# Kernel tuning notes

Measured on AMD Instinct MI355X. Metric: run time of the kernel, lower is better.

Reference implementation:

```python
import jax, jax.numpy as jnp
import numpy as np

N_NODES = 50000


def setup_inputs() -> dict:
    key = jax.random.key(0)
    k1, k2, k3, k4 = jax.random.split(key, 4)
    N, E, D_IN, D_OUT = N_NODES, 1_600_000, 128, 128
    x = jax.random.normal(k1, (N, D_IN), dtype=jnp.float32)
    edge_index = jax.random.randint(k2, (2, E), 0, N, dtype=jnp.int64)
    W = jax.random.normal(k3, (D_IN, D_OUT), dtype=jnp.float32) * (1.0 / np.sqrt(D_IN))
    b = jax.random.normal(k4, (D_OUT,), dtype=jnp.float32) * 0.01
    return {"x": x, "edge_index": edge_index, "W": W, "b": b}


def reference(x, edge_index, W, b):
    N = x.shape[0]
    # add self loops: edge (i, i) for every node
    loops = jnp.arange(N, dtype=edge_index.dtype)
    row = jnp.concatenate([edge_index[0], loops])  # [E+N]
    col = jnp.concatenate([edge_index[1], loops])  # [E+N]
    # degree over col (matches torch_geometric degree(col, N))
    deg = jax.ops.segment_sum(jnp.ones_like(col, dtype=x.dtype), col, num_segments=N)
    deg_inv_sqrt = jnp.where(deg > 0, jax.lax.rsqrt(jnp.maximum(deg, 1.0)), 0.0)
    norm = deg_inv_sqrt[row] * deg_inv_sqrt[col]  # [E+N]
    # linear transform then gather-multiply-scatter (segment sum over row)
    xl = x @ W + b  # [N, D_OUT]
    msg = norm[:, None] * xl[col]  # [E+N, D_OUT]
    out = jax.ops.segment_sum(msg, row, num_segments=N)
    return out
```

## Files before the change

kernel.cpp:

```cpp
#include <hip/hip_runtime.h>
#include <hip/hip_bf16.h>


#define D     128
#define TILE  8192
#define BINB  1024
#define RPB   128
#define MAXB  512
#define SPLIT_CAP 8192

typedef short  bf16x8 __attribute__((ext_vector_type(8)));
typedef float  f32x4  __attribute__((ext_vector_type(4)));
typedef unsigned short us4 __attribute__((ext_vector_type(4)));
typedef unsigned short us8 __attribute__((ext_vector_type(8)));

static __device__ __forceinline__ unsigned short f2bf(float f) {
    unsigned u = __float_as_uint(f);
    u = (u + 0x7FFFu + ((u >> 16) & 1u)) >> 16;
    return (unsigned short)u;
}
static __device__ __forceinline__ float bf2f(unsigned short s) {
    return __uint_as_float(((unsigned)s) << 16);
}

__global__ __launch_bounds__(256) void k_prep(const float* __restrict__ W,
                                              unsigned short* __restrict__ wtb,
                                              int* __restrict__ bcur,
                                              int* __restrict__ bcurC,
                                              int NB, int CAP, int CAPC) {
    int i = blockIdx.x * 256 + threadIdx.x;
    if (i < NB) { bcur[i] = i * CAP; bcurC[i] = i * CAPC; }
    if (i < D * D) {
        int n = i >> 7, k = i & 127;
        wtb[n * 128 + k] = f2bf(W[k * 128 + n]);
    }
}

__global__ __launch_bounds__(1024) void k_binjoint(
        const int* __restrict__ rows, const int* __restrict__ cols,
        int* __restrict__ bcur, int* __restrict__ bcurC,
        unsigned* __restrict__ ebuf, unsigned char* __restrict__ cebuf,
        const float* __restrict__ x, const unsigned short* __restrict__ wtb,
        const float* __restrict__ bia, unsigned short* __restrict__ xlb,
        int E, int N, int NB, int CAP, int CAPC, int NT) {
    __shared__ __align__(16) unsigned char smem[65536];
    const int t = threadIdx.x;

    if ((int)blockIdx.x >= NT) {
        unsigned short (*wt)[136] = (unsigned short (*)[136])smem;
        unsigned short (*xs)[136] = (unsigned short (*)[136])(smem + 34816);
        const int row0 = ((int)blockIdx.x - NT) * 64;
        #pragma unroll
        for (int i = 0; i < 2; ++i) {
            int j = i * 1024 + t;
            int n = j >> 4, k8 = j & 15;
            us8 v = *(const us8*)&wtb[j * 8];
            *(us8*)&wt[n][k8 * 8] = v;
        }
        #pragma unroll
        for (int i = 0; i < 2; ++i) {
            int j = i * 1024 + t;
            int r = j >> 5, c4 = j & 31;
            int gr = row0 + r;
            us4 o = (us4){0, 0, 0, 0};
            if (gr < N) {
                float4 v = *(const float4*)&x[(size_t)gr * D + c4 * 4];
                o = (us4){f2bf(v.x), f2bf(v.y), f2bf(v.z), f2bf(v.w)};
            }
            *(us4*)&xs[r][c4 * 4] = o;
        }
        __syncthreads();
        if (t < 256) {
            const int w  = t >> 6, l = t & 63;
            const int m0 = w * 16;
            const int lm = l & 15, lq = l >> 4;
            f32x4 acc[8];
            #pragma unroll
            for (int nt = 0; nt < 8; ++nt) acc[nt] = (f32x4){0.f, 0.f, 0.f, 0.f};
            #pragma unroll
            for (int kk = 0; kk < 4; ++kk) {
                const int kof = kk * 32 + lq * 8;
                bf16x8 a = *(const bf16x8*)&xs[m0 + lm][kof];
                #pragma unroll
                for (int nt = 0; nt < 8; ++nt) {
                    bf16x8 bb = *(const bf16x8*)&wt[nt * 16 + lm][kof];
                    acc[nt] = __builtin_amdgcn_mfma_f32_16x16x32_bf16(a, bb, acc[nt], 0, 0, 0);
                }
            }
            #pragma unroll
            for (int nt = 0; nt < 8; ++nt) {
                const int col = nt * 16 + lm;
                const float bc = bia[col];
                #pragma unroll
                for (int r = 0; r < 4; ++r) {
                    int grow = row0 + m0 + lq * 4 + r;
                    if (grow < N) xlb[(size_t)grow * D + col] = f2bf(acc[nt][r] + bc);
                }
            }
        }
        return;
    }

    unsigned*       sorted  = (unsigned*)smem;
    unsigned short* sortedC = (unsigned short*)(smem + 32768);
    int* lcnt   = (int*)(smem + 49152);
    int* lbase  = lcnt + 512;
    int* excl   = lcnt + 1024;
    int* cur    = lcnt + 1536;
    int* lcntC  = lcnt + 2048;
    int* lbaseC = lcnt + 2560;
    int* exclC  = lcnt + 3072;
    int* curC   = lcnt + 3584;

    const int base = blockIdx.x * TILE;
    int m = E - base; if (m > TILE) m = TILE;

    unsigned p[TILE / BINB];
    unsigned short q[TILE / BINB];
    #pragma unroll
    for (int it = 0; it < TILE / BINB; ++it) {
        int i = it * BINB + t;
        if (i < m) {
            unsigned r = (unsigned)rows[base + i];
            unsigned c = (unsigned)cols[base + i];
            p[it] = c | ((r & 127u) << 16) | ((r >> 7) << 23);
            q[it] = (unsigned short)c;
        }
    }
    if (t < 512) { lcnt[t] = 0; lcntC[t] = 0; }
    __syncthreads();
    #pragma unroll
    for (int it = 0; it < TILE / BINB; ++it) {
        int i = it * BINB + t;
        if (i < m) {
            atomicAdd(&lcnt[p[it] >> 23], 1);
            atomicAdd(&lcntC[q[it] >> 7], 1);
        }
    }
    __syncthreads();
    if (t < 64) {
        int k0 = t * 8, v[8], s = 0;
        #pragma unroll
        for (int u = 0; u < 8; ++u) { v[u] = lcnt[k0 + u]; s += v[u]; }
        int inc = s;
        #pragma unroll
        for (int off = 1; off < 64; off <<= 1) { int o = __shfl_up(inc, off); if (t >= off) inc += o; }
        int run = inc - s;
        #pragma unroll
        for (int u = 0; u < 8; ++u) { excl[k0 + u] = run; cur[k0 + u] = run; run += v[u]; }
    } else if (t < 128) {
        int l = t - 64, k0 = l * 8, v[8], s = 0;
        #pragma unroll
        for (int u = 0; u < 8; ++u) { v[u] = lcntC[k0 + u]; s += v[u]; }
        int inc = s;
        #pragma unroll
        for (int off = 1; off < 64; off <<= 1) { int o = __shfl_up(inc, off); if (l >= off) inc += o; }
        int run = inc - s;
        #pragma unroll
        for (int u = 0; u < 8; ++u) { exclC[k0 + u] = run; curC[k0 + u] = run; run += v[u]; }
    }
    for (int b = t; b < NB; b += BINB) {
        int c = lcnt[b];
        lbase[b] = c ? atomicAdd(&bcur[b], c) : 0;
        int cc = lcntC[b];
        lbaseC[b] = cc ? atomicAdd(&bcurC[b], cc) : 0;
    }
    __syncthreads();
    #pragma unroll
    for (int it = 0; it < TILE / BINB; ++it) {
        int i = it * BINB + t;
        if (i < m) {
            int pos  = atomicAdd(&cur[p[it] >> 23], 1);
            sorted[pos] = p[it];
            int posC = atomicAdd(&curC[q[it] >> 7], 1);
            sortedC[posC] = q[it];
        }
    }
    __syncthreads();
    #pragma unroll
    for (int it = 0; it < TILE / BINB; ++it) {
        int i = it * BINB + t;
        if (i < m) {
            unsigned pp = sorted[i];
            int bk = pp >> 23;
            int g  = lbase[bk] + i - excl[bk];
            if (g < (bk + 1) * CAP) ebuf[g] = pp & 0x7FFFFFu;
            unsigned short qq = sortedC[i];
            int bc = qq >> 7;
            int gc = lbaseC[bc] + i - exclC[bc];
            if (gc < (bc + 1) * CAPC) cebuf[gc] = (unsigned char)(qq & 127u);
        }
    }
}

__global__ __launch_bounds__(1024) void k_split(const int* __restrict__ bcur,
                                                const int* __restrict__ bcurC,
                                                const unsigned* __restrict__ ebuf,
                                                const unsigned char* __restrict__ cebuf,
                                                unsigned short* __restrict__ ecol,
                                                int* __restrict__ begN,
                                                int* __restrict__ endN,
                                                float* __restrict__ dis,
                                                int N, int CAP, int CAPC) {
    __shared__ unsigned short sorted[SPLIT_CAP];
    __shared__ int cnt[RPB];
    __shared__ int excl[RPB];
    __shared__ int cur[RPB];
    __shared__ int cntD[RPB];
    const int b = blockIdx.x, t = threadIdx.x;
    const int base = b * CAP;
    int m = bcur[b] - base; if (m > CAP) m = CAP;
    const int baseC = b * CAPC;
    int mD = bcurC[b] - baseC; if (mD > CAPC) mD = CAPC;
    if (t < RPB) { cnt[t] = 0; cntD[t] = 0; }
    __syncthreads();
    const unsigned* cw = (const unsigned*)(cebuf + baseC);
    int nw = mD >> 2;
    for (int i = t; i < nw; i += 1024) {
        unsigned u = cw[i];
        atomicAdd(&cntD[u & 255u], 1);
        atomicAdd(&cntD[(u >> 8) & 255u], 1);
        atomicAdd(&cntD[(u >> 16) & 255u], 1);
        atomicAdd(&cntD[u >> 24], 1);
    }
    if (t < (mD & 3)) atomicAdd(&cntD[cebuf[baseC + nw * 4 + t]], 1);
    for (int i = t; i < m; i += 1024)
        atomicAdd(&cnt[(ebuf[base + i] >> 16) & 127], 1);
    __syncthreads();
    const int row0 = b * RPB;
    if (t < RPB && row0 + t < N)
        dis[row0 + t] = rsqrtf((float)(cntD[t] + 1));
    if (t < 64) {
        int v0 = cnt[2 * t], v1 = cnt[2 * t + 1];
        int s = v0 + v1, inc = s;
        #pragma unroll
        for (int off = 1; off < 64; off <<= 1) { int o = __shfl_up(inc, off); if (t >= off) inc += o; }
        int ex = inc - s;
        excl[2 * t] = ex;          cur[2 * t] = ex;
        excl[2 * t + 1] = ex + v0; cur[2 * t + 1] = ex + v0;
    }
    __syncthreads();
    if (t < RPB && row0 + t < N) {
        begN[row0 + t] = base + excl[t];
        endN[row0 + t] = base + excl[t] + cnt[t];
    }
    for (int i = t; i < m; i += 1024) {
        unsigned p = ebuf[base + i];
        int pos = atomicAdd(&cur[(p >> 16) & 127], 1);
        sorted[pos] = (unsigned short)(p & 0xFFFFu);
    }
    __syncthreads();
    for (int i = t; i < m; i += 1024)
        ecol[base + i] = sorted[i];
}

__global__ __launch_bounds__(256) void k_reduce(const int* __restrict__ begN,
                                                const int* __restrict__ endN,
                                                const unsigned short* __restrict__ ecol,
                                                const float* __restrict__ dis,
                                                const unsigned short* __restrict__ xlb,
                                                float* __restrict__ out, int N) {
    const int wave = threadIdx.x >> 6;
    const int lane = threadIdx.x & 63;
    const int i = blockIdx.x * 4 + wave;
    if (i >= N) return;
    const float di = dis[i];

    const ushort2 sv = *reinterpret_cast<const ushort2*>(xlb + (size_t)i * D + lane * 2);
    float ax = di * di * bf2f(sv.x);
    float ay = di * di * bf2f(sv.y);

    const int beg = begN[i], end = endN[i];
    for (int base = beg; base < end; base += 64) {
        int m = end - base; if (m > 64) m = 64;
        int   c = 0;
        float n = 0.0f;
        if (lane < m) {
            c = ecol[base + lane];
            n = di * dis[c];
        }
        for (int j = 0; j < m; j += 8) {
            float vx[8], vy[8], nn[8];
            #pragma unroll
            for (int u = 0; u < 8; ++u) {
                int cc = __shfl(c, j + u);
                ushort2 s = *reinterpret_cast<const ushort2*>(xlb + (size_t)cc * D + lane * 2);
                vx[u] = bf2f(s.x);
                vy[u] = bf2f(s.y);
                nn[u] = __shfl(n, j + u);
            }
            #pragma unroll
            for (int u = 0; u < 8; ++u) {
                ax = fmaf(nn[u], vx[u], ax);
                ay = fmaf(nn[u], vy[u], ay);
            }
        }
    }
    *reinterpret_cast<float2*>(out + (size_t)i * D + lane * 2) = make_float2(ax, ay);
}

__global__ __launch_bounds__(256) void k_zero(int* __restrict__ p, int n) {
    int i = blockIdx.x * 256 + threadIdx.x;
    if (i < n) p[i] = 0;
}
__global__ __launch_bounds__(256) void k_deg(const int* __restrict__ cols,
                                             int* __restrict__ cntc, int E) {
    int e = blockIdx.x * 256 + threadIdx.x;
    if (e < E) atomicAdd(&cntc[cols[e]], 1);
}
__global__ __launch_bounds__(256) void k_dis(const int* __restrict__ cntc,
                                             float* __restrict__ dis, int N) {
    int i = blockIdx.x * 256 + threadIdx.x;
    if (i < N) dis[i] = rsqrtf((float)(cntc[i] + 1));
}
#define GEMM_R 8
__global__ __launch_bounds__(128) void k_gemmf(const float* __restrict__ x,
                                               const float* __restrict__ W,
                                               const float* __restrict__ b,
                                               float* __restrict__ xl, int N) {
    __shared__ float xs[GEMM_R][D];
    const int c  = threadIdx.x;
    const int r0 = blockIdx.x * GEMM_R;
    #pragma unroll
    for (int r = 0; r < GEMM_R; ++r) {
        int row = r0 + r;
        xs[r][c] = (row < N) ? x[row * D + c] : 0.0f;
    }
    __syncthreads();
    float acc[GEMM_R];
    const float bc = b[c];
    #pragma unroll
    for (int r = 0; r < GEMM_R; ++r) acc[r] = bc;
    for (int k = 0; k < D; k += 4) {
        const float w0 = W[(k + 0) * D + c];
        const float w1 = W[(k + 1) * D + c];
        const float w2 = W[(k + 2) * D + c];
        const float w3 = W[(k + 3) * D + c];
        #pragma unroll
        for (int r = 0; r < GEMM_R; ++r) {
            const float4 xv = *reinterpret_cast<const float4*>(&xs[r][k]);
            acc[r] = fmaf(xv.x, w0, acc[r]);
            acc[r] = fmaf(xv.y, w1, acc[r]);
            acc[r] = fmaf(xv.z, w2, acc[r]);
            acc[r] = fmaf(xv.w, w3, acc[r]);
        }
    }
    #pragma unroll
    for (int r = 0; r < GEMM_R; ++r) {
        int row = r0 + r;
        if (row < N) xl[row * D + c] = acc[r];
    }
}
__global__ __launch_bounds__(256) void k_self(const float* __restrict__ xl,
                                              const float* __restrict__ dis,
                                              float* __restrict__ out, int N) {
    int gid = blockIdx.x * 256 + threadIdx.x;
    int i = gid >> 7;
    if (i < N) {
        float d = dis[i];
        out[gid] = d * d * xl[gid];
    }
}
__global__ __launch_bounds__(256) void k_scatter(const int* __restrict__ rows,
                                                 const int* __restrict__ cols,
                                                 const float* __restrict__ dis,
                                                 const float* __restrict__ xl,
                                                 float* __restrict__ out, int E) {
    long long gid = (long long)blockIdx.x * 256 + threadIdx.x;
    int e    = (int)(gid >> 6);
    int lane = (int)(gid & 63);
    if (e >= E) return;
    const int row = rows[e];
    const int col = cols[e];
    const float nrm = dis[row] * dis[col];
    atomicAdd(&out[row * D + lane],      nrm * xl[col * D + lane]);
    atomicAdd(&out[row * D + 64 + lane], nrm * xl[col * D + 64 + lane]);
}

extern "C" void kernel_launch(void* const* d_in, const int* in_sizes, int n_in,
                              void* d_out, int out_size, void* d_ws, size_t ws_size,
                              hipStream_t stream) {
    const float* x   = (const float*)d_in[0];
    const int*   ei  = (const int*)d_in[1];
    const float* W   = (const float*)d_in[2];
    const float* b   = (const float*)d_in[3];
    float*       out = (float*)d_out;

    const int N = in_sizes[0] / D;
    const int E = in_sizes[1] / 2;
    const int* rows = ei;
    const int* cols = ei + E;
    const int NB = (N + RPB - 1) / RPB;
    const int NT = (E + TILE - 1) / TILE;
    const int GN = (N + 63) / 64;
    const int CAP  = (((2 * E) / NB) + 63) / 64 * 64;
    const int CAPC = CAP;

    char* p = (char*)d_ws;
    size_t off = 0;
    unsigned short* xlb   = (unsigned short*)(p + off); off += (size_t)N * D * 2;
    unsigned short* wtb   = (unsigned short*)(p + off); off += (size_t)D * D * 2;
    float*          dis   = (float*)(p + off);          off += (size_t)N * 4;
    int*            bcur  = (int*)(p + off);            off += (size_t)MAXB * 4;
    int*            bcurC = (int*)(p + off);            off += (size_t)MAXB * 4;
    int*            begN  = (int*)(p + off);            off += (size_t)N * 4;
    int*            endN  = (int*)(p + off);            off += (size_t)N * 4;
    unsigned*       ebuf  = (unsigned*)(p + off);       off += (size_t)NB * CAP * 4;
    unsigned short* ecol  = (unsigned short*)(p + off); off += (size_t)NB * CAP * 2;
    unsigned char*  cebuf = (unsigned char*)(p + off);  off += (size_t)NB * CAPC;

    const int gN = (N + 255) / 256;
    const int gE = (E + 255) / 256;

    if (N <= 65536 && NB <= MAXB && CAP <= SPLIT_CAP && ws_size >= off) {
        k_prep    <<<(D * D + 255) / 256, 256, 0, stream>>>(W, wtb, bcur, bcurC, NB, CAP, CAPC);
        k_binjoint<<<NT + GN, BINB, 0, stream>>>(rows, cols, bcur, bcurC, ebuf, cebuf,
                                                 x, wtb, b, xlb, E, N, NB, CAP, CAPC, NT);
        k_split   <<<NB, 1024, 0, stream>>>(bcur, bcurC, ebuf, cebuf, ecol, begN, endN, dis, N, CAP, CAPC);
        k_reduce  <<<(N + 3) / 4, 256, 0, stream>>>(begN, endN, ecol, dis, xlb, out, N);
    } else {
        char* q = (char*)d_ws;
        float* xl   = (float*)q;
        float* disF = (float*)(q + (size_t)N * D * 4);
        int*   cc   = (int*)(q + (size_t)N * D * 4 + (size_t)N * 4);
        k_zero <<<gN, 256, 0, stream>>>(cc, N);
        k_deg  <<<gE, 256, 0, stream>>>(cols, cc, E);
        k_dis  <<<gN, 256, 0, stream>>>(cc, disF, N);
        k_gemmf<<<(N + GEMM_R - 1) / GEMM_R, 128, 0, stream>>>(x, W, b, xl, N);
        k_self <<<((N * D) + 255) / 256, 256, 0, stream>>>(xl, disF, out, N);
        long long st = (long long)E * 64;
        k_scatter<<<(int)((st + 255) / 256), 256, 0, stream>>>(rows, cols, disF, xl, out, E);
    }
}
```

Baseline: 159.2 us.

## Prescale xl rows by deg^-1/2 in split and restructure reduce gather

```diff
diff --git a/kernel.cpp b/kernel.cpp
--- a/kernel.cpp
+++ b/kernel.cpp
@@ -201,12 +201,14 @@
                                                 int* __restrict__ begN,
                                                 int* __restrict__ endN,
                                                 float* __restrict__ dis,
+                                                unsigned short* __restrict__ xlb,
                                                 int N, int CAP, int CAPC) {
     __shared__ unsigned short sorted[SPLIT_CAP];
     __shared__ int cnt[RPB];
     __shared__ int excl[RPB];
     __shared__ int cur[RPB];
     __shared__ int cntD[RPB];
+    __shared__ float sdis[RPB];
     const int b = blockIdx.x, t = threadIdx.x;
     const int base = b * CAP;
     int m = bcur[b] - base; if (m > CAP) m = CAP;
@@ -228,8 +230,11 @@
         atomicAdd(&cnt[(ebuf[base + i] >> 16) & 127], 1);
     __syncthreads();
     const int row0 = b * RPB;
-    if (t < RPB && row0 + t < N)
-        dis[row0 + t] = rsqrtf((float)(cntD[t] + 1));
+    if (t < RPB) {
+        float dv = rsqrtf((float)(cntD[t] + 1));
+        sdis[t] = dv;
+        if (row0 + t < N) dis[row0 + t] = dv;
+    }
     if (t < 64) {
         int v0 = cnt[2 * t], v1 = cnt[2 * t + 1];
         int s = v0 + v1, inc = s;
@@ -248,6 +253,21 @@
         unsigned p = ebuf[base + i];
         int pos = atomicAdd(&cur[(p >> 16) & 127], 1);
         sorted[pos] = (unsigned short)(p & 0xFFFFu);
+    }
+    #pragma unroll
+    for (int k = 0; k < 2; ++k) {
+        int j = k * 1024 + t;
+        int r = j >> 4, e8 = j & 15;
+        int gr = row0 + r;
+        if (gr < N) {
+            unsigned short* px = &xlb[(size_t)gr * D + e8 * 8];
+            us8 v = *(const us8*)px;
+            float dv = sdis[r];
+            us8 o;
+            #pragma unroll
+            for (int qq = 0; qq < 8; ++qq) o[qq] = f2bf(dv * bf2f(v[qq]));
+            *(us8*)px = o;
+        }
     }
     __syncthreads();
     for (int i = t; i < m; i += 1024)
@@ -262,41 +282,72 @@
                                                 float* __restrict__ out, int N) {
     const int wave = threadIdx.x >> 6;
     const int lane = threadIdx.x & 63;
+    const int half = lane >> 5;
+    const int l32  = lane & 31;
     const int i = blockIdx.x * 4 + wave;
     if (i >= N) return;
-    const float di = dis[i];
-
-    const ushort2 sv = *reinterpret_cast<const ushort2*>(xlb + (size_t)i * D + lane * 2);
-    float ax = di * di * bf2f(sv.x);
-    float ay = di * di * bf2f(sv.y);
-
+
+    float a0, a1, a2, a3;
+    {
+        us4 sv = *(const us4*)&xlb[(size_t)i * D + (l32 << 2)];
+        float s = (half == 0) ? 1.0f : 0.0f;
+        a0 = s * bf2f(sv[0]); a1 = s * bf2f(sv[1]);
+        a2 = s * bf2f(sv[2]); a3 = s * bf2f(sv[3]);
+    }
     const int beg = begN[i], end = endN[i];
+
+#define FETCH(V, J) do { \
+    _Pragma("unroll") \
+    for (int u = 0; u < 8; ++u) { \
+        int cc = __shfl(c, (J) + 2 * u + half); \
+        V[u] = *(const us4*)&xlb[((size_t)cc << 7) + (l32 << 2)]; \
+    } } while (0)
+#define CFULL(V) do { \
+    _Pragma("unroll") \
+    for (int u = 0; u < 8; ++u) { \
+        a0 += bf2f(V[u][0]); a1 += bf2f(V[u][1]); \
+        a2 += bf2f(V[u][2]); a3 += bf2f(V[u][3]); \
+    } } while (0)
+#define CTAIL(V, J) do { \
+    _Pragma("unroll") \
+    for (int u = 0; u < 8; ++u) { \
+        float w = ((J) + 2 * u + half < m) ? 1.0f : 0.0f; \
+        a0 = fmaf(w, bf2f(V[u][0]), a0); a1 = fmaf(w, bf2f(V[u][1]), a1); \
+        a2 = fmaf(w, bf2f(V[u][2]), a2); a3 = fmaf(w, bf2f(V[u][3]), a3); \
+    } } while (0)
+
     for (int base = beg; base < end; base += 64) {
         int m = end - base; if (m > 64) m = 64;
-        int   c = 0;
-        float n = 0.0f;
-        if (lane < m) {
-            c = ecol[base + lane];
-            n = di * dis[c];
-        }
-        for (int j = 0; j < m; j += 8) {
-            float vx[8], vy[8], nn[8];
-            #pragma unroll
-            for (int u = 0; u < 8; ++u) {
-                int cc = __shfl(c, j + u);
-                ushort2 s = *reinterpret_cast<const ushort2*>(xlb + (size_t)cc * D + lane * 2);
-                vx[u] = bf2f(s.x);
-                vy[u] = bf2f(s.y);
-                nn[u] = __shfl(n, j + u);
-            }
-            #pragma unroll
-            for (int u = 0; u < 8; ++u) {
-                ax = fmaf(nn[u], vx[u], ax);
-                ay = fmaf(nn[u], vy[u], ay);
-            }
-        }
-    }
-    *reinterpret_cast<float2*>(out + (size_t)i * D + lane * 2) = make_float2(ax, ay);
+        int c = 0;
+        if (lane < m) c = ecol[base + lane];
+        us4 A[8], B[8];
+        int j = 0;
+        FETCH(A, 0);
+        for (; j + 32 <= m; j += 32) {
+            FETCH(B, j + 16);
+            CFULL(A);
+            if (j + 32 < m) FETCH(A, j + 32);
+            CFULL(B);
+        }
+        int rem = m - j;
+        if (rem > 0) {
+            if (rem > 16) { FETCH(B, j + 16); CFULL(A); CTAIL(B, j + 16); }
+            else          { CTAIL(A, j); }
+        }
+    }
+#undef FETCH
+#undef CFULL
+#undef CTAIL
+
+    a0 += __shfl_xor(a0, 32);
+    a1 += __shfl_xor(a1, 32);
+    a2 += __shfl_xor(a2, 32);
+    a3 += __shfl_xor(a3, 32);
+    if (half == 0) {
+        const float di = dis[i];
+        *(float4*)&out[(size_t)i * D + (l32 << 2)] =
+            make_float4(di * a0, di * a1, di * a2, di * a3);
+    }
 }
 
 __global__ __launch_bounds__(256) void k_zero(int* __restrict__ p, int n) {
@@ -416,7 +467,7 @@
         k_prep    <<<(D * D + 255) / 256, 256, 0, stream>>>(W, wtb, bcur, bcurC, NB, CAP, CAPC);
         k_binjoint<<<NT + GN, BINB, 0, stream>>>(rows, cols, bcur, bcurC, ebuf, cebuf,
                                                  x, wtb, b, xlb, E, N, NB, CAP, CAPC, NT);
-        k_split   <<<NB, 1024, 0, stream>>>(bcur, bcurC, ebuf, cebuf, ecol, begN, endN, dis, N, CAP, CAPC);
+        k_split   <<<NB, 1024, 0, stream>>>(bcur, bcurC, ebuf, cebuf, ecol, begN, endN, dis, xlb, N, CAP, CAPC);
         k_reduce  <<<(N + 3) / 4, 256, 0, stream>>>(begN, endN, ecol, dis, xlb, out, N);
     } else {
         char* q = (char*)d_ws;
```

Result: slower. 164.0 us (+3.0%).
